# Optimization experiments

Measured on AMD Instinct MI355X. Metric: run time of the kernel, lower is better.

Reference implementation:

```python
import jax, jax.numpy as jnp
import numpy as np

B, N, C_IN, C_OUT, K = 2, 2048, 64, 128, 3
SCALE = 12.0  # spread points over ~12^3 unit voxels (voxel_size = 1.0 in the module)


def setup_inputs() -> dict:
    key = jax.random.key(0)
    k1, k2, k3 = jax.random.split(key, 3)
    points = jax.random.uniform(k1, (B, N, 3), dtype=jnp.float32) * SCALE
    features = jax.random.normal(k2, (B, N, C_IN), dtype=jnp.float32)
    # kaiming-uniform-ish init for weight viewed as (K^3*Cin, Cout)
    fan_in = K * K * K * C_IN
    bound = np.sqrt(6.0 / fan_in)
    weight = jax.random.uniform(k3, (K, K, K, C_IN, C_OUT), dtype=jnp.float32,
                                minval=-bound, maxval=bound)
    bias = jnp.zeros((C_OUT,), dtype=jnp.float32)
    return {"points": points, "features": features, "weight": weight, "bias": bias}


def reference(points, features, weight, bias):
    """Sparse 3D conv over a unit voxel grid.

    For each point i, every point j whose voxel index differs by an offset
    within the KxKxK stencil contributes features[j] @ weight[rel_offset].
    Vectorized as: per-offset boolean match matrix (B,N,N) -> masked
    feature aggregation -> one GEMM with that offset's (Cin,Cout) kernel slice.
    """
    k = weight.shape[0]
    c = k // 2
    # torch's .long() truncates toward zero; jnp astype(int32) does the same for floats
    vox = points.astype(jnp.int32)  # (B, N, 3)
    out = jnp.zeros(features.shape[:2] + (weight.shape[-1],), dtype=features.dtype)
    for oi in range(k):
        for oj in range(k):
            for ok in range(k):
                off = jnp.array([oi - c, oj - c, ok - c], dtype=jnp.int32)
                target = vox + off  # voxel that neighbor j must occupy for center i
                # mask[b, i, j] = all(vox[b, j] == vox[b, i] + off)
                mask = jnp.all(vox[:, None, :, :] == target[:, :, None, :], axis=-1)
                agg = jnp.einsum('bij,bjc->bic', mask.astype(features.dtype), features)
                out = out + agg @ weight[oi, oj, ok]  # (B,N,Cin)@(Cin,Cout)
    return out + bias
```

## Files before the change

### kernel.cpp

```cpp
#include <hip/hip_runtime.h>

#define BATCH 2
#define NPTS  2048
#define CIN   64
#define COUT  128
#define GD    14
#define GD2   (GD*GD)
#define NCELL (GD*GD*GD)
#define M     (BATCH*NPTS)
#define VOXF  (BATCH*NCELL*CIN)
#define WTEL  (27*COUT*CIN)

typedef __bf16 bf16x8 __attribute__((ext_vector_type(8)));
typedef float  f32x4  __attribute__((ext_vector_type(4)));
typedef unsigned short us8 __attribute__((ext_vector_type(8)));

__device__ __forceinline__ unsigned short f2bf(float f) {
    unsigned u = __builtin_bit_cast(unsigned, f);
    return (unsigned short)((u + 0x7FFFu + ((u >> 16) & 1u)) >> 16);
}

__global__ __launch_bounds__(256) void k_init(const float* __restrict__ points,
                                              const float* __restrict__ weight,
                                              float* __restrict__ voxgrid,
                                              int* __restrict__ cellid,
                                              unsigned short* __restrict__ wT) {
    int idx = blockIdx.x * 256 + threadIdx.x;
    if (idx < VOXF/4) ((float4*)voxgrid)[idx] = make_float4(0.f, 0.f, 0.f, 0.f);
    if (idx < M) {
        int vx = (int)points[idx*3 + 0];
        int vy = (int)points[idx*3 + 1];
        int vz = (int)points[idx*3 + 2];
        cellid[idx] = (vx + 1)*GD2 + (vy + 1)*GD + (vz + 1);
    }
    if (idx < WTEL) {
        int off = idx >> 13;
        int rem = idx & 8191;
        int n   = rem >> 6;
        int k   = rem & 63;
        wT[idx] = f2bf(weight[off*8192 + k*128 + n]);
    }
}

__global__ __launch_bounds__(256) void k_scatter(const float* __restrict__ feat,
                                                 const int* __restrict__ cellid,
                                                 float* __restrict__ voxgrid) {
    int idx = blockIdx.x * 256 + threadIdx.x;
    int g   = idx >> 6;
    int cin = idx & 63;
    int b   = g >> 11;
    atomicAdd(&voxgrid[((size_t)b*NCELL + cellid[g])*CIN + cin], feat[idx]);
}

__global__ __launch_bounds__(256) void k_gemm(const float* __restrict__ voxgrid,
                                              const int* __restrict__ cellid,
                                              const unsigned short* __restrict__ wT,
                                              const float* __restrict__ bias,
                                              float* __restrict__ out) {
    static constexpr int DELTA[27] = {
        -211,-210,-209,-197,-196,-195,-183,-182,-181,
         -15, -14, -13,  -1,   0,   1,  13,  14,  15,
         181, 182, 183, 195, 196, 197, 209, 210, 211 };

    __shared__ unsigned short Abuf[16*72];

    const int t   = threadIdx.x;
    const int g0  = blockIdx.x * 16;
    const int b   = g0 >> 11;

    const int row = t >> 4;
    const int c4  = (t & 15) * 4;
    const int cell = cellid[g0 + row];
    const float* aptr = voxgrid + ((size_t)b*NCELL + cell)*CIN + c4;

    const int l   = t & 63;
    const int w   = t >> 6;
    const int q   = l >> 4;
    const int col = l & 15;
    const int n0  = blockIdx.y * 64 + w * 16;
    const unsigned short* wt0 = wT + (size_t)(n0 + col)*CIN + q*8;
    const unsigned short* abase = &Abuf[(l & 15)*72 + q*8];

    f32x4 acc = {0.f, 0.f, 0.f, 0.f};

    float4 v  = *(const float4*)(aptr + DELTA[0]*CIN);
    us8    b0 = *(const us8*)(wt0);
    us8    b1 = *(const us8*)(wt0 + 32);

    #pragma unroll
    for (int oo = 0; oo < 27; ++oo) {
        __syncthreads();
        ushort4 pk;
        pk.x = f2bf(v.x); pk.y = f2bf(v.y); pk.z = f2bf(v.z); pk.w = f2bf(v.w);
        *(ushort4*)&Abuf[row*72 + c4] = pk;
        __syncthreads();

        if (oo < 26) {
            v  = *(const float4*)(aptr + DELTA[oo+1]*CIN);
        }
        us8 b0n, b1n;
        if (oo < 26) {
            b0n = *(const us8*)(wt0 + (oo+1)*8192);
            b1n = *(const us8*)(wt0 + (oo+1)*8192 + 32);
        }

        us8 a0 = *(const us8*)(abase);
        us8 a1 = *(const us8*)(abase + 32);
        acc = __builtin_amdgcn_mfma_f32_16x16x32_bf16(
                  __builtin_bit_cast(bf16x8, a0), __builtin_bit_cast(bf16x8, b0), acc, 0, 0, 0);
        acc = __builtin_amdgcn_mfma_f32_16x16x32_bf16(
                  __builtin_bit_cast(bf16x8, a1), __builtin_bit_cast(bf16x8, b1), acc, 0, 0, 0);

        if (oo < 26) { b0 = b0n; b1 = b1n; }
    }

    const float bs = bias[n0 + col];
    #pragma unroll
    for (int r = 0; r < 4; ++r) {
        out[(size_t)(g0 + q*4 + r)*COUT + n0 + col] = acc[r] + bs;
    }
}

extern "C" void kernel_launch(void* const* d_in, const int* in_sizes, int n_in,
                              void* d_out, int out_size, void* d_ws, size_t ws_size,
                              hipStream_t stream) {
    (void)in_sizes; (void)n_in; (void)out_size; (void)ws_size;
    const float* points   = (const float*)d_in[0];
    const float* features = (const float*)d_in[1];
    const float* weight   = (const float*)d_in[2];
    const float* bias     = (const float*)d_in[3];
    float* out = (float*)d_out;

    float*          voxgrid = (float*)d_ws;
    int*            cellid  = (int*)((char*)d_ws + (size_t)VOXF*4);
    unsigned short* wTp     = (unsigned short*)((char*)d_ws + (size_t)VOXF*4 + (size_t)M*4);

    k_init<<<(WTEL + 255)/256, 256, 0, stream>>>(points, weight, voxgrid, cellid, wTp);
    k_scatter<<<(M*CIN + 255)/256, 256, 0, stream>>>(features, cellid, voxgrid);
    dim3 grid(M/16, 2, 1);
    k_gemm<<<grid, 256, 0, stream>>>(voxgrid, cellid, wTp, bias, out);
}
```

Baseline: 81.37 us.

## Fuse scatter into prep kernel and drop LDS staging in gather-GEMM

Merges the init and scatter kernels into one prep kernel that computes cell ids, atomically scatters features and transposes weights, with the grid zeroing moved to hipMemsetAsync. The GEMM kernel stops staging A through shared memory with two barriers per offset; each lane now loads its own fp32 A fragment directly and converts it in registers, using a 4-deep register prefetch ring for A and B. This removes a kernel launch and all per-offset syncthreads. In exchange it adds register pressure and redundant A loads across the four waves of a block.

New measurement: 103.4 us. 1.27x slower.

```diff
diff --git a/kernel.cpp b/kernel.cpp
--- a/kernel.cpp
+++ b/kernel.cpp
@@ -20,36 +20,37 @@
     return (unsigned short)((u + 0x7FFFu + ((u >> 16) & 1u)) >> 16);
 }
 
-__global__ __launch_bounds__(256) void k_init(const float* __restrict__ points,
+__device__ __forceinline__ bf16x8 cvt8(f32x4 lo, f32x4 hi) {
+    bf16x8 r;
+    r[0] = (__bf16)lo[0]; r[1] = (__bf16)lo[1]; r[2] = (__bf16)lo[2]; r[3] = (__bf16)lo[3];
+    r[4] = (__bf16)hi[0]; r[5] = (__bf16)hi[1]; r[6] = (__bf16)hi[2]; r[7] = (__bf16)hi[3];
+    return r;
+}
+
+__global__ __launch_bounds__(256) void k_prep(const float* __restrict__ points,
+                                              const float* __restrict__ feat,
                                               const float* __restrict__ weight,
                                               float* __restrict__ voxgrid,
                                               int* __restrict__ cellid,
                                               unsigned short* __restrict__ wT) {
-    int idx = blockIdx.x * 256 + threadIdx.x;
-    if (idx < VOXF/4) ((float4*)voxgrid)[idx] = make_float4(0.f, 0.f, 0.f, 0.f);
-    if (idx < M) {
-        int vx = (int)points[idx*3 + 0];
-        int vy = (int)points[idx*3 + 1];
-        int vz = (int)points[idx*3 + 2];
-        cellid[idx] = (vx + 1)*GD2 + (vy + 1)*GD + (vz + 1);
+    const int i   = blockIdx.x * 256 + threadIdx.x;
+    const int g   = i >> 6;
+    const int cin = i & 63;
+    const int b   = g >> 11;
+
+    const int vx = (int)points[g*3 + 0];
+    const int vy = (int)points[g*3 + 1];
+    const int vz = (int)points[g*3 + 2];
+    const int cell = (vx + 1)*GD2 + (vy + 1)*GD + (vz + 1);
+    if (cin == 0) cellid[g] = cell;
+    atomicAdd(&voxgrid[((size_t)b*NCELL + cell)*CIN + cin], feat[i]);
+
+    if (i < WTEL) {
+        const int off = i >> 13;
+        const int k   = (i >> 7) & 63;
+        const int n   = i & 127;
+        wT[off*8192 + n*64 + k] = f2bf(weight[i]);
     }
-    if (idx < WTEL) {
-        int off = idx >> 13;
-        int rem = idx & 8191;
-        int n   = rem >> 6;
-        int k   = rem & 63;
-        wT[idx] = f2bf(weight[off*8192 + k*128 + n]);
-    }
-}
-
-__global__ __launch_bounds__(256) void k_scatter(const float* __restrict__ feat,
-                                                 const int* __restrict__ cellid,
-                                                 float* __restrict__ voxgrid) {
-    int idx = blockIdx.x * 256 + threadIdx.x;
-    int g   = idx >> 6;
-    int cin = idx & 63;
-    int b   = g >> 11;
-    atomicAdd(&voxgrid[((size_t)b*NCELL + cellid[g])*CIN + cin], feat[idx]);
 }
 
 __global__ __launch_bounds__(256) void k_gemm(const float* __restrict__ voxgrid,
@@ -61,64 +62,63 @@
         -211,-210,-209,-197,-196,-195,-183,-182,-181,
          -15, -14, -13,  -1,   0,   1,  13,  14,  15,
          181, 182, 183, 195, 196, 197, 209, 210, 211 };
+    constexpr int PF = 4;
 
-    __shared__ unsigned short Abuf[16*72];
+    const int bid  = blockIdx.x;
+    const int t    = threadIdx.x;
+    const int tile = bid & 255;
+    const int half = bid >> 8;
+    const int g0   = tile * 16;
+    const int b    = g0 >> 11;
+    const int l    = t & 63;
+    const int w    = t >> 6;
+    const int q    = l >> 4;
+    const int col  = l & 15;
+    const int n0   = half * 64 + w * 16;
 
-    const int t   = threadIdx.x;
-    const int g0  = blockIdx.x * 16;
-    const int b   = g0 >> 11;
+    const int cell = cellid[g0 + col];
+    const float* arow = voxgrid + ((size_t)b*NCELL + cell)*CIN + q*8;
+    const unsigned short* wt = wT + (size_t)(n0 + col)*CIN + q*8;
 
-    const int row = t >> 4;
-    const int c4  = (t & 15) * 4;
-    const int cell = cellid[g0 + row];
-    const float* aptr = voxgrid + ((size_t)b*NCELL + cell)*CIN + c4;
-
-    const int l   = t & 63;
-    const int w   = t >> 6;
-    const int q   = l >> 4;
-    const int col = l & 15;
-    const int n0  = blockIdx.y * 64 + w * 16;
-    const unsigned short* wt0 = wT + (size_t)(n0 + col)*CIN + q*8;
-    const unsigned short* abase = &Abuf[(l & 15)*72 + q*8];
+    f32x4 av[PF][4];
+    us8   bv[PF][2];
+    #pragma unroll
+    for (int s = 0; s < PF; ++s) {
+        const float* p = arow + DELTA[s]*CIN;
+        av[s][0] = *(const f32x4*)(p);
+        av[s][1] = *(const f32x4*)(p + 4);
+        av[s][2] = *(const f32x4*)(p + 32);
+        av[s][3] = *(const f32x4*)(p + 36);
+        bv[s][0] = *(const us8*)(wt + s*8192);
+        bv[s][1] = *(const us8*)(wt + s*8192 + 32);
+    }
 
     f32x4 acc = {0.f, 0.f, 0.f, 0.f};
-
-    float4 v  = *(const float4*)(aptr + DELTA[0]*CIN);
-    us8    b0 = *(const us8*)(wt0);
-    us8    b1 = *(const us8*)(wt0 + 32);
-
     #pragma unroll
     for (int oo = 0; oo < 27; ++oo) {
-        __syncthreads();
-        ushort4 pk;
-        pk.x = f2bf(v.x); pk.y = f2bf(v.y); pk.z = f2bf(v.z); pk.w = f2bf(v.w);
-        *(ushort4*)&Abuf[row*72 + c4] = pk;
-        __syncthreads();
-
-        if (oo < 26) {
-            v  = *(const float4*)(aptr + DELTA[oo+1]*CIN);
+        const int slot = oo % PF;
+        bf16x8 a0 = cvt8(av[slot][0], av[slot][1]);
+        bf16x8 a1 = cvt8(av[slot][2], av[slot][3]);
+        us8 b0 = bv[slot][0], b1 = bv[slot][1];
+        if (oo + PF < 27) {
+            const float* p = arow + DELTA[oo+PF]*CIN;
+            av[slot][0] = *(const f32x4*)(p);
+            av[slot][1] = *(const f32x4*)(p + 4);
+            av[slot][2] = *(const f32x4*)(p + 32);
+            av[slot][3] = *(const f32x4*)(p + 36);
+            bv[slot][0] = *(const us8*)(wt + (oo+PF)*8192);
+            bv[slot][1] = *(const us8*)(wt + (oo+PF)*8192 + 32);
         }
-        us8 b0n, b1n;
-        if (oo < 26) {
-            b0n = *(const us8*)(wt0 + (oo+1)*8192);
-            b1n = *(const us8*)(wt0 + (oo+1)*8192 + 32);
-        }
-
-        us8 a0 = *(const us8*)(abase);
-        us8 a1 = *(const us8*)(abase + 32);
         acc = __builtin_amdgcn_mfma_f32_16x16x32_bf16(
-                  __builtin_bit_cast(bf16x8, a0), __builtin_bit_cast(bf16x8, b0), acc, 0, 0, 0);
+                  a0, __builtin_bit_cast(bf16x8, b0), acc, 0, 0, 0);
         acc = __builtin_amdgcn_mfma_f32_16x16x32_bf16(
-                  __builtin_bit_cast(bf16x8, a1), __builtin_bit_cast(bf16x8, b1), acc, 0, 0, 0);
-
-        if (oo < 26) { b0 = b0n; b1 = b1n; }
+                  a1, __builtin_bit_cast(bf16x8, b1), acc, 0, 0, 0);
     }
 
     const float bs = bias[n0 + col];
     #pragma unroll
-    for (int r = 0; r < 4; ++r) {
+    for (int r = 0; r < 4; ++r)
         out[(size_t)(g0 + q*4 + r)*COUT + n0 + col] = acc[r] + bs;
-    }
 }
 
 extern "C" void kernel_launch(void* const* d_in, const int* in_sizes, int n_in,
@@ -131,12 +131,12 @@
     const float* bias     = (const float*)d_in[3];
     float* out = (float*)d_out;
 
-    float*          voxgrid = (float*)d_ws;
-    int*            cellid  = (int*)((char*)d_ws + (size_t)VOXF*4);
-    unsigned short* wTp     = (unsigned short*)((char*)d_ws + (size_t)VOXF*4 + (size_t)M*4);
+    char* ws = (char*)d_ws;
+    float*          voxgrid = (float*)ws;           ws += (size_t)VOXF*4;
+    int*            cellid  = (int*)ws;             ws += (size_t)M*4;
+    unsigned short* wTp     = (unsigned short*)ws;
 
-    k_init<<<(WTEL + 255)/256, 256, 0, stream>>>(points, weight, voxgrid, cellid, wTp);
-    k_scatter<<<(M*CIN + 255)/256, 256, 0, stream>>>(features, cellid, voxgrid);
-    dim3 grid(M/16, 2, 1);
-    k_gemm<<<grid, 256, 0, stream>>>(voxgrid, cellid, wTp, bias, out);
+    hipMemsetAsync(voxgrid, 0, (size_t)VOXF*4, stream);
+    k_prep<<<(M*CIN)/256, 256, 0, stream>>>(points, features, weight, voxgrid, cellid, wTp);
+    k_gemm<<<512, 256, 0, stream>>>(voxgrid, cellid, wTp, bias, out);
 }
```
